# Kernel optimization log

Measured on AMD Instinct MI355X. Metric: run time of the kernel, lower is better.

## Reference

```python
import jax, jax.numpy as jnp
import numpy as np

B, S, H = 4, 2048, 1024

def setup_inputs() -> dict:
    key = jax.random.key(0)
    ks = jax.random.split(key, 4)
    scale = 1.0 / np.sqrt(H)
    x = jax.random.normal(ks[0], (B, S, H), dtype=jnp.float32)
    Wq = jax.random.normal(ks[1], (H, H), dtype=jnp.float32) * scale
    Wk = jax.random.normal(ks[2], (H, H), dtype=jnp.float32) * scale
    Wv = jax.random.normal(ks[3], (H, H), dtype=jnp.float32) * scale
    bq = jnp.zeros((H,), dtype=jnp.float32)
    bk = jnp.zeros((H,), dtype=jnp.float32)
    bv = jnp.zeros((H,), dtype=jnp.float32)
    return {"x": x, "Wq": Wq, "bq": bq, "Wk": Wk, "bk": bk, "Wv": Wv, "bv": bv}

def reference(x, Wq, bq, Wk, bk, Wv, bv):
    # Linear: y = x @ W^T + b (torch nn.Linear convention)
    Q = jnp.einsum('bsh,oh->bso', x, Wq) + bq
    K = jnp.einsum('bsh,oh->bso', x, Wk) + bk
    V = jnp.einsum('bsh,oh->bso', x, Wv) + bv
    scores = jnp.einsum('bqh,bkh->bqk', Q, K) / jnp.sqrt(jnp.float32(H))
    attn = jax.nn.softmax(scores, axis=-1)
    return jnp.einsum('bqk,bkh->bqh', attn, V)
```

## Files before the change

kernel.cpp:

```cpp
#include <hip/hip_runtime.h>
#include <cstdint>
#include <cstddef>


typedef __bf16 bf16;
typedef _Float16 f16;
typedef __bf16 bf16x8 __attribute__((ext_vector_type(8)));
typedef __bf16 bf16x4 __attribute__((ext_vector_type(4)));
typedef float f32x4 __attribute__((ext_vector_type(4)));

#define LDS_TOTAL 131072

#define XO (8388608 / 8)
#define WO (1048576 / 8)
__global__ __launch_bounds__(256)
void cvt_all(const float* __restrict__ x, const float* __restrict__ Wq,
             const float* __restrict__ Wk, const float* __restrict__ Wv,
             bf16* __restrict__ xb, bf16* __restrict__ Wqkv,
             float* __restrict__ rsum)
{
    const int i = blockIdx.x * 256 + threadIdx.x;
    if (i < 2048) {
        f32x4 zz = {0.f, 0.f, 0.f, 0.f};
        ((f32x4*)rsum)[i] = zz;
    }
    const float* src;
    bf16* dst;
    if (i < XO) {
        src = x + 8 * (size_t)i;
        dst = xb + 8 * (size_t)i;
    } else {
        const int j = i - XO;
        const int w = j / WO;
        const int off = j - w * WO;
        const float* ws_ = (w == 0) ? Wq : (w == 1) ? Wk : Wv;
        src = ws_ + 8 * (size_t)off;
        dst = Wqkv + 8 * (size_t)j;
    }
    f32x4 v0 = *(const f32x4*)src;
    f32x4 v1 = *(const f32x4*)(src + 4);
    bf16x8 o;
#pragma unroll
    for (int r = 0; r < 4; ++r) { o[r] = (bf16)v0[r]; o[4 + r] = (bf16)v1[r]; }
    *(bf16x8*)dst = o;
}

#define BM1 128
#define BN1 128
#define BK1 64

__device__ __forceinline__ void stage_tile(const bf16* __restrict__ g, int ld,
                                           bf16* lds_generic, int tid)
{
    auto lds3 = (__attribute__((address_space(3))) char*)lds_generic;
    const int wave = tid >> 6;
#pragma unroll
    for (int issue = 0; issue < 4; ++issue) {
        const int p   = issue * 256 + tid;
        const int row = p >> 3;
        const int cp  = p & 7;
        const int c   = cp ^ (row & 7);
        const bf16* gp = g + (size_t)row * ld + c * 8;
        const unsigned wave_base = (unsigned)(issue * 4096 + wave * 1024);
        __builtin_amdgcn_global_load_lds(
            (const __attribute__((address_space(1))) void*)gp,
            (__attribute__((address_space(3))) void*)(lds3 + wave_base),
            16, 0, 0);
    }
}

__device__ __forceinline__ bf16x8 read_frag(const bf16* lds, int row, int chunk)
{
    const int cp = chunk ^ (row & 7);
    return *(const bf16x8*)(lds + row * BK1 + cp * 8);
}

__global__ __launch_bounds__(256, 2)
void gemm_qkv(const bf16* __restrict__ A, const bf16* __restrict__ Bm,
              const float* __restrict__ bias0, const float* __restrict__ bias1,
              const float* __restrict__ bias2, bf16* __restrict__ C, int K)
{
    __shared__ alignas(16) bf16 As[2][BM1 * BK1];
    __shared__ alignas(16) bf16 Bs[2][BN1 * BK1];

    const int tid  = threadIdx.x;
    const int lane = tid & 63;
    const int wid  = tid >> 6;
    const int wr   = (wid >> 1) * 64;
    const int wc   = (wid & 1) * 64;
    const int quad = lane >> 4;
    const int l16  = lane & 15;

    {
    }
    const unsigned gx = gridDim.x;
    unsigned flat = blockIdx.x + gx * blockIdx.y;
    const unsigned chunk = (gx * gridDim.y) >> 3;
    flat = (flat & 7u) * chunk + (flat >> 3);
    const int bx = flat % gx;
    const int by = flat / gx;

    const int m0 = by * BM1;
    const int n0 = bx * BN1;

    const bf16* Ab = A + (size_t)m0 * K;
    const bf16* Bb = Bm + (size_t)n0 * K;

    f32x4 acc[4][4] = {};

    stage_tile(Ab, K, As[0], tid);
    stage_tile(Bb, K, Bs[0], tid);

    const int niter = K / BK1;
    for (int it = 0; it < niter; ++it) {
        const int cur = it & 1;
        __syncthreads();
        if (it + 1 < niter) {
            stage_tile(Ab + (it + 1) * BK1, K, As[cur ^ 1], tid);
            stage_tile(Bb + (it + 1) * BK1, K, Bs[cur ^ 1], tid);
        }
#pragma unroll
        for (int h = 0; h < 2; ++h) {
            bf16x8 af[4], bfr[4];
#pragma unroll
            for (int i = 0; i < 4; ++i)
                af[i]  = read_frag(As[cur], wr + i * 16 + l16, h * 4 + quad);
#pragma unroll
            for (int j = 0; j < 4; ++j)
                bfr[j] = read_frag(Bs[cur], wc + j * 16 + l16, h * 4 + quad);
#pragma unroll
            for (int i = 0; i < 4; ++i)
#pragma unroll
                for (int j = 0; j < 4; ++j)
                    acc[i][j] = __builtin_amdgcn_mfma_f32_16x16x32_bf16(
                        af[i], bfr[j], acc[i][j], 0, 0, 0);
        }
    }

#pragma unroll
    for (int j = 0; j < 4; ++j) {
        const int col3 = n0 + wc + j * 16 + l16;
#pragma unroll
        for (int i = 0; i < 4; ++i) {
            const int rbase = m0 + wr + i * 16 + quad * 4;
            const int mat = col3 >> 10;
            const int col = col3 & 1023;
            const float* bp = (mat == 0) ? bias0 : (mat == 1) ? bias1 : bias2;
            const float bj = bp[col];
            if (mat < 2) {
                bf16* Cb = C + (size_t)mat * (8u << 20);
#pragma unroll
                for (int r = 0; r < 4; ++r)
                    Cb[(size_t)(rbase + r) * 1024 + col] =
                        (bf16)(acc[i][j][r] + bj);
            } else {
                bf16* Cb = C + (size_t)(16u << 20);
                const int b = rbase >> 11;
                const int s = rbase & 2047;
                bf16x4 tmp;
#pragma unroll
                for (int r = 0; r < 4; ++r) tmp[r] = (bf16)(acc[i][j][r] + bj);
                *(bf16x4*)(Cb + (((size_t)((b << 10) + col)) << 11) + s) = tmp;
            }
        }
    }
}

template <int OUTMODE, int NW_N>
__global__ __launch_bounds__(512, 2)
void gemm256(const bf16* __restrict__ A, const bf16* __restrict__ Bm,
             void* __restrict__ C, float* __restrict__ rsum,
             int K, int N, float alpha, long zA, long zB, long zC)
{
    constexpr int MI = 2 * NW_N;
    extern __shared__ __align__(16) char smem[];
    auto lds3 = (__attribute__((address_space(3))) char*)smem;

    const int tid  = threadIdx.x;
    const int lane = tid & 63;
    const int wid  = tid >> 6;
    const int quad = lane >> 4;
    const int l16  = lane & 15;
    const int wc   = (wid % NW_N) * 64;
    const int wr   = (wid / NW_N) * (MI * 16);

    const unsigned gx = gridDim.x, gy = gridDim.y;
    unsigned flat = blockIdx.x + gx * (blockIdx.y + gy * blockIdx.z);
    const unsigned chunk = (gx * gy * gridDim.z) >> 3;
    flat = (flat & 7u) * chunk + (flat >> 3);
    const int bx = flat % gx;
    const unsigned r2 = flat / gx;
    const int by = r2 % gy;
    const int z  = r2 / gy;

    const int m0 = by * 256;
    const int n0 = bx * (NW_N * 64);

    const bf16* Ab = A + (size_t)z * zA + (size_t)m0 * K;
    const bf16* Bb = Bm + (size_t)z * zB + (size_t)n0 * K;

    const int sr  = tid >> 3;
    const int sc  = (tid & 7) ^ (sr & 7);
    const size_t soff = (size_t)sr * K + (size_t)sc * 8;
    const long  hstep = 64L * K;
    const long  h1off = 128L * K;
    const unsigned dmabase = (unsigned)(wid * 1024);

#define STAGE(g, ldsoff)                                                       \
    do {                                                                       \
        __builtin_amdgcn_global_load_lds(                                      \
            (const __attribute__((address_space(1))) void*)((g) + soff),       \
            (__attribute__((address_space(3))) void*)(lds3 + (ldsoff) + dmabase), \
            16, 0, 0);                                                         \
        __builtin_amdgcn_global_load_lds(                                      \
            (const __attribute__((address_space(1))) void*)((g) + soff + hstep), \
            (__attribute__((address_space(3))) void*)(lds3 + (ldsoff) + 8192 + dmabase), \
            16, 0, 0);                                                         \
    } while (0)

    const char* pa = (const char*)smem + (wr + l16) * 128;
    const int x0 = (quad ^ (l16 & 7)) * 16;

    const int NT = K / 64;
    f32x4 acc[MI][4] = {};

    if constexpr (NW_N == 4) {
        const char* pb = (const char*)smem + 65536 + (wc + l16) * 128;
        bf16x8 af[4][2], b01[2][2], b23[2][2];

        STAGE(Ab, 0u);           STAGE(Ab + h1off, 16384u);
        STAGE(Bb, 65536u);       STAGE(Bb + h1off, 65536u + 16384u);
        STAGE(Ab + 64, 32768u);  STAGE(Ab + 64 + h1off, 32768u + 16384u);
        asm volatile("s_waitcnt vmcnt(4)\n\ts_barrier" ::: "memory");

        for (int t = 0; t < NT; ++t) {
            const unsigned d  = (unsigned)(t & 1) * 32768u;
            const unsigned dn = 32768u - d;
            const char* paT = pa + d;
            const char* pbT = pb + d;

#pragma unroll
            for (int i = 0; i < 4; ++i) {
                af[i][0] = *(const bf16x8*)(paT + i * 2048 + x0);
                af[i][1] = *(const bf16x8*)(paT + i * 2048 + (x0 ^ 64));
            }
#pragma unroll
            for (int j = 0; j < 2; ++j) {
                b01[j][0] = *(const bf16x8*)(pbT + j * 2048 + x0);
                b01[j][1] = *(const bf16x8*)(pbT + j * 2048 + (x0 ^ 64));
            }
            if (t + 1 < NT) STAGE(Bb + (t + 1) * 64, 65536u + dn);
            __builtin_amdgcn_s_setprio(1);
#pragma unroll
            for (int i = 0; i < 4; ++i)
#pragma unroll
                for (int j = 0; j < 2; ++j) {
                    acc[i][j] = __builtin_amdgcn_mfma_f32_16x16x32_bf16(
                        af[i][0], b01[j][0], acc[i][j], 0, 0, 0);
                    acc[i][j] = __builtin_amdgcn_mfma_f32_16x16x32_bf16(
                        af[i][1], b01[j][1], acc[i][j], 0, 0, 0);
                }
            __builtin_amdgcn_s_setprio(0);

#pragma unroll
            for (int j = 0; j < 2; ++j) {
                b23[j][0] = *(const bf16x8*)(pbT + (2 + j) * 2048 + x0);
                b23[j][1] = *(const bf16x8*)(pbT + (2 + j) * 2048 + (x0 ^ 64));
            }
            if (t + 1 < NT) STAGE(Bb + (t + 1) * 64 + h1off, 65536u + dn + 16384u);
            __builtin_amdgcn_s_setprio(1);
#pragma unroll
            for (int i = 0; i < 4; ++i)
#pragma unroll
                for (int j = 0; j < 2; ++j) {
                    acc[i][2 + j] = __builtin_amdgcn_mfma_f32_16x16x32_bf16(
                        af[i][0], b23[j][0], acc[i][2 + j], 0, 0, 0);
                    acc[i][2 + j] = __builtin_amdgcn_mfma_f32_16x16x32_bf16(
                        af[i][1], b23[j][1], acc[i][2 + j], 0, 0, 0);
                }
            __builtin_amdgcn_s_setprio(0);

#pragma unroll
            for (int i = 0; i < 4; ++i) {
                af[i][0] = *(const bf16x8*)(paT + (4 + i) * 2048 + x0);
                af[i][1] = *(const bf16x8*)(paT + (4 + i) * 2048 + (x0 ^ 64));
            }
            __builtin_amdgcn_s_setprio(1);
#pragma unroll
            for (int i = 0; i < 4; ++i)
#pragma unroll
                for (int j = 0; j < 2; ++j) {
                    acc[4 + i][2 + j] = __builtin_amdgcn_mfma_f32_16x16x32_bf16(
                        af[i][0], b23[j][0], acc[4 + i][2 + j], 0, 0, 0);
                    acc[4 + i][2 + j] = __builtin_amdgcn_mfma_f32_16x16x32_bf16(
                        af[i][1], b23[j][1], acc[4 + i][2 + j], 0, 0, 0);
                }
            __builtin_amdgcn_s_setprio(0);

            asm volatile("s_barrier" ::: "memory");

#pragma unroll
            for (int j = 0; j < 2; ++j) {
                b01[j][0] = *(const bf16x8*)(pbT + j * 2048 + x0);
                b01[j][1] = *(const bf16x8*)(pbT + j * 2048 + (x0 ^ 64));
            }
            if (t + 2 < NT) {
                STAGE(Ab + (t + 2) * 64, d);
                STAGE(Ab + (t + 2) * 64 + h1off, d + 16384u);
            }
            __builtin_amdgcn_s_setprio(1);
#pragma unroll
            for (int i = 0; i < 4; ++i)
#pragma unroll
                for (int j = 0; j < 2; ++j) {
                    acc[4 + i][j] = __builtin_amdgcn_mfma_f32_16x16x32_bf16(
                        af[i][0], b01[j][0], acc[4 + i][j], 0, 0, 0);
                    acc[4 + i][j] = __builtin_amdgcn_mfma_f32_16x16x32_bf16(
                        af[i][1], b01[j][1], acc[4 + i][j], 0, 0, 0);
                }
            __builtin_amdgcn_s_setprio(0);

            if (t + 2 < NT)
                asm volatile("s_waitcnt vmcnt(4)\n\ts_barrier" ::: "memory");
            else if (t + 1 < NT)
                asm volatile("s_waitcnt vmcnt(0)\n\ts_barrier" ::: "memory");
        }
    } else {
        bf16x8 af[2][2], bfr[4][2];

        STAGE(Ab, 0u);           STAGE(Ab + h1off, 16384u);
        STAGE(Bb, 98304u);
        STAGE(Ab + 64, 32768u);  STAGE(Ab + 64 + h1off, 32768u + 16384u);
        asm volatile("s_waitcnt vmcnt(4)\n\ts_barrier" ::: "memory");

        for (int t = 0; t < NT; ++t) {
            const char* paT = pa + (unsigned)(t % 3) * 32768u;
            const char* pbT = (const char*)smem + 98304u +
                              (unsigned)(t & 1) * 16384u + (wc + l16) * 128;

#pragma unroll
            for (int i = 0; i < 2; ++i) {
                af[i][0] = *(const bf16x8*)(paT + i * 2048 + x0);
                af[i][1] = *(const bf16x8*)(paT + i * 2048 + (x0 ^ 64));
            }
#pragma unroll
            for (int j = 0; j < 4; ++j) {
                bfr[j][0] = *(const bf16x8*)(pbT + j * 2048 + x0);
                bfr[j][1] = *(const bf16x8*)(pbT + j * 2048 + (x0 ^ 64));
            }
            if (t + 1 < NT)
                STAGE(Bb + (t + 1) * 64, 98304u + (unsigned)((t + 1) & 1) * 16384u);
            __builtin_amdgcn_s_setprio(1);
#pragma unroll
            for (int i = 0; i < 2; ++i)
#pragma unroll
                for (int j = 0; j < 4; ++j) {
                    acc[i][j] = __builtin_amdgcn_mfma_f32_16x16x32_bf16(
                        af[i][0], bfr[j][0], acc[i][j], 0, 0, 0);
                    acc[i][j] = __builtin_amdgcn_mfma_f32_16x16x32_bf16(
                        af[i][1], bfr[j][1], acc[i][j], 0, 0, 0);
                }
            __builtin_amdgcn_s_setprio(0);

#pragma unroll
            for (int i = 0; i < 2; ++i) {
                af[i][0] = *(const bf16x8*)(paT + (2 + i) * 2048 + x0);
                af[i][1] = *(const bf16x8*)(paT + (2 + i) * 2048 + (x0 ^ 64));
            }
            if (t + 2 < NT) {
                const unsigned da = (unsigned)((t + 2) % 3) * 32768u;
                STAGE(Ab + (t + 2) * 64, da);
                STAGE(Ab + (t + 2) * 64 + h1off, da + 16384u);
            }
            __builtin_amdgcn_s_setprio(1);
#pragma unroll
            for (int i = 0; i < 2; ++i)
#pragma unroll
                for (int j = 0; j < 4; ++j) {
                    acc[2 + i][j] = __builtin_amdgcn_mfma_f32_16x16x32_bf16(
                        af[i][0], bfr[j][0], acc[2 + i][j], 0, 0, 0);
                    acc[2 + i][j] = __builtin_amdgcn_mfma_f32_16x16x32_bf16(
                        af[i][1], bfr[j][1], acc[2 + i][j], 0, 0, 0);
                }
            __builtin_amdgcn_s_setprio(0);

            if (t + 2 < NT)
                asm volatile("s_waitcnt vmcnt(4)\n\ts_barrier" ::: "memory");
            else if (t + 1 < NT)
                asm volatile("s_waitcnt vmcnt(0)\n\ts_barrier" ::: "memory");
        }
    }
#undef STAGE

    if constexpr (OUTMODE == 5) {
        float psum[8][4];
#pragma unroll
        for (int i = 0; i < 8; ++i)
#pragma unroll
            for (int r = 0; r < 4; ++r) psum[i][r] = 0.f;

        bf16* Pb = (bf16*)C + (size_t)z * zC;
#pragma unroll
        for (int j = 0; j < 4; ++j) {
            const int col3 = n0 + wc + j * 16 + l16;
#pragma unroll
            for (int i = 0; i < MI; ++i) {
                const int rbase = m0 + wr + i * 16 + quad * 4;
#pragma unroll
                for (int r = 0; r < 4; ++r) {
                    const float p = __expf(acc[i][j][r] * alpha);
                    Pb[(size_t)(rbase + r) * N + col3] = (bf16)p;
                    psum[i][r] += p;
                }
            }
        }
#pragma unroll
        for (int i = 0; i < MI; ++i)
#pragma unroll
            for (int r = 0; r < 4; ++r) {
#pragma unroll
                for (int o = 1; o < 16; o <<= 1)
                    psum[i][r] += __shfl_xor(psum[i][r], o, 64);
            }
        if (l16 == 0) {
            float* rs = rsum + (size_t)z * 2048;
#pragma unroll
            for (int i = 0; i < MI; ++i) {
                const int rbase = m0 + wr + i * 16 + quad * 4;
#pragma unroll
                for (int r = 0; r < 4; ++r)
                    atomicAdd(&rs[rbase + r], psum[i][r]);
            }
        }
    } else {
        const float* rs = rsum + (size_t)z * 2048;
#pragma unroll
        for (int j = 0; j < 4; ++j) {
            const int col3 = n0 + wc + j * 16 + l16;
#pragma unroll
            for (int i = 0; i < MI; ++i) {
                const int rbase = m0 + wr + i * 16 + quad * 4;
                float* Cf = (float*)C + (size_t)z * zC;
#pragma unroll
                for (int r = 0; r < 4; ++r)
                    Cf[(size_t)(rbase + r) * N + col3] =
                        acc[i][j][r] * (1.0f / rs[rbase + r]);
            }
        }
    }
}

extern "C" void kernel_launch(void* const* d_in, const int* in_sizes, int n_in,
                              void* d_out, int out_size, void* d_ws, size_t ws_size,
                              hipStream_t stream)
{
    constexpr int B = 4, S = 2048, H = 1024;
    const float* x  = (const float*)d_in[0];
    const float* Wq = (const float*)d_in[1];
    const float* bq = (const float*)d_in[2];
    const float* Wk = (const float*)d_in[3];
    const float* bk = (const float*)d_in[4];
    const float* Wv = (const float*)d_in[5];
    const float* bv = (const float*)d_in[6];
    float* out = (float*)d_out;

    char* ws = (char*)d_ws;
    bf16* xb    = (bf16*)ws;
    bf16* Wqkv  = (bf16*)(ws + (size_t)(16 << 20));
    float* rsum = (float*)(ws + (size_t)(22 << 20));
    bf16* Q     = (bf16*)(ws + (size_t)(24 << 20));
    bf16* Kp    = (bf16*)(ws + (size_t)(40 << 20));
    bf16* Vt    = (bf16*)(ws + (size_t)(56 << 20));
    bf16* P     = (bf16*)(ws + (size_t)(72 << 20));

    static bool attr_done = false;
    if (!attr_done) {
        attr_done = true;
        (void)hipFuncSetAttribute(reinterpret_cast<const void*>(gemm256<5, 4>),
                                  hipFuncAttributeMaxDynamicSharedMemorySize,
                                  LDS_TOTAL);
        (void)hipFuncSetAttribute(reinterpret_cast<const void*>(gemm256<6, 2>),
                                  hipFuncAttributeMaxDynamicSharedMemorySize,
                                  LDS_TOTAL);
    }

    dim3 blk(256, 1, 1);
    dim3 blk512(512, 1, 1);

    cvt_all<<<dim3((XO + 3 * WO) / 256), blk, 0, stream>>>(
        x, Wq, Wk, Wv, xb, Wqkv, rsum);

    gemm_qkv<<<dim3(3 * H / BN1, (B * S) / BM1, 1), blk, 0, stream>>>(
        xb, Wqkv, bq, bk, bv, Q, H);

    gemm256<5, 4><<<dim3(S / 256, S / 256, B), blk512, LDS_TOTAL, stream>>>(
        Q, Kp, P, rsum, H, S, 0.03125f,
        (long)S * H, (long)S * H, (long)S * S);

    gemm256<6, 2><<<dim3(H / 128, S / 256, B), blk512, LDS_TOTAL, stream>>>(
        P, Vt, out, rsum, S, H, 1.0f,
        (long)S * S, (long)H * S, (long)S * H);
}
```

Baseline: 237.9 us.

## Fuse QK^T-softmax and PV GEMMs into one kernel with per-row-group spin barrier

Merges the score/exp GEMM and the P·V GEMM into a single persistent-style kernel of 256 blocks. Each block computes one 256x256 score tile, adds its partial row sums atomically, then spin-waits on a per-row-group counter until all 8 column tiles are done before computing its 256x128 output tile. This removes a kernel launch and the tail between the two GEMMs, and keeps P hot in L2. It relies on all 256 blocks being co-resident, at two per CU, or the spin barrier deadlocks. The QKV GEMM also drops its block-index swizzle.

```diff
diff --git a/kernel.cpp b/kernel.cpp
--- a/kernel.cpp
+++ b/kernel.cpp
@@ -4,7 +4,6 @@
 
 
 typedef __bf16 bf16;
-typedef _Float16 f16;
 typedef __bf16 bf16x8 __attribute__((ext_vector_type(8)));
 typedef __bf16 bf16x4 __attribute__((ext_vector_type(4)));
 typedef float f32x4 __attribute__((ext_vector_type(4)));
@@ -17,13 +16,12 @@
 void cvt_all(const float* __restrict__ x, const float* __restrict__ Wq,
              const float* __restrict__ Wk, const float* __restrict__ Wv,
              bf16* __restrict__ xb, bf16* __restrict__ Wqkv,
-             float* __restrict__ rsum)
+             float* __restrict__ rsum, unsigned* __restrict__ cnt)
 {
     const int i = blockIdx.x * 256 + threadIdx.x;
-    if (i < 2048) {
-        f32x4 zz = {0.f, 0.f, 0.f, 0.f};
-        ((f32x4*)rsum)[i] = zz;
-    }
+    f32x4 zz = {0.f, 0.f, 0.f, 0.f};
+    if (i < 2048) ((f32x4*)rsum)[i] = zz;
+    if (i < 8)    ((f32x4*)(void*)cnt)[i] = zz;
     const float* src;
     bf16* dst;
     if (i < XO) {
@@ -91,17 +89,8 @@
     const int quad = lane >> 4;
     const int l16  = lane & 15;
 
-    {
-    }
-    const unsigned gx = gridDim.x;
-    unsigned flat = blockIdx.x + gx * blockIdx.y;
-    const unsigned chunk = (gx * gridDim.y) >> 3;
-    flat = (flat & 7u) * chunk + (flat >> 3);
-    const int bx = flat % gx;
-    const int by = flat / gx;
-
-    const int m0 = by * BM1;
-    const int n0 = bx * BN1;
+    const int m0 = blockIdx.y * BM1;
+    const int n0 = blockIdx.x * BN1;
 
     const bf16* Ab = A + (size_t)m0 * K;
     const bf16* Bb = Bm + (size_t)n0 * K;
@@ -166,13 +155,12 @@
     }
 }
 
-template <int OUTMODE, int NW_N>
 __global__ __launch_bounds__(512, 2)
-void gemm256(const bf16* __restrict__ A, const bf16* __restrict__ Bm,
-             void* __restrict__ C, float* __restrict__ rsum,
-             int K, int N, float alpha, long zA, long zB, long zC)
+void attn_fused(const bf16* __restrict__ Qg, const bf16* __restrict__ Kg,
+                const bf16* __restrict__ Vtg, bf16* __restrict__ Pg,
+                float* __restrict__ rsum, unsigned* __restrict__ cnt,
+                float* __restrict__ out)
 {
-    constexpr int MI = 2 * NW_N;
     extern __shared__ __align__(16) char smem[];
     auto lds3 = (__attribute__((address_space(3))) char*)smem;
 
@@ -181,56 +169,53 @@
     const int wid  = tid >> 6;
     const int quad = lane >> 4;
     const int l16  = lane & 15;
-    const int wc   = (wid % NW_N) * 64;
-    const int wr   = (wid / NW_N) * (MI * 16);
-
-    const unsigned gx = gridDim.x, gy = gridDim.y;
+
+    const unsigned gx = 8, gy = 8;
     unsigned flat = blockIdx.x + gx * (blockIdx.y + gy * blockIdx.z);
-    const unsigned chunk = (gx * gy * gridDim.z) >> 3;
-    flat = (flat & 7u) * chunk + (flat >> 3);
+    flat = (flat & 7u) * 32u + (flat >> 3);
     const int bx = flat % gx;
     const unsigned r2 = flat / gx;
     const int by = r2 % gy;
     const int z  = r2 / gy;
-
-    const int m0 = by * 256;
-    const int n0 = bx * (NW_N * 64);
-
-    const bf16* Ab = A + (size_t)z * zA + (size_t)m0 * K;
-    const bf16* Bb = Bm + (size_t)z * zB + (size_t)n0 * K;
-
-    const int sr  = tid >> 3;
-    const int sc  = (tid & 7) ^ (sr & 7);
-    const size_t soff = (size_t)sr * K + (size_t)sc * 8;
-    const long  hstep = 64L * K;
-    const long  h1off = 128L * K;
+    const int grp = z * 8 + by;
+
+    const int sr = tid >> 3;
+    const int sc = (tid & 7) ^ (sr & 7);
     const unsigned dmabase = (unsigned)(wid * 1024);
-
-#define STAGE(g, ldsoff)                                                       \
+    const int x0 = (quad ^ (l16 & 7)) * 16;
+
+#define STAGE(g, soff, hstep, ldsoff)                                          \
     do {                                                                       \
         __builtin_amdgcn_global_load_lds(                                      \
-            (const __attribute__((address_space(1))) void*)((g) + soff),       \
+            (const __attribute__((address_space(1))) void*)((g) + (soff)),     \
             (__attribute__((address_space(3))) void*)(lds3 + (ldsoff) + dmabase), \
             16, 0, 0);                                                         \
         __builtin_amdgcn_global_load_lds(                                      \
-            (const __attribute__((address_space(1))) void*)((g) + soff + hstep), \
+            (const __attribute__((address_space(1))) void*)((g) + (soff) + (hstep)), \
             (__attribute__((address_space(3))) void*)(lds3 + (ldsoff) + 8192 + dmabase), \
             16, 0, 0);                                                         \
     } while (0)
 
-    const char* pa = (const char*)smem + (wr + l16) * 128;
-    const int x0 = (quad ^ (l16 & 7)) * 16;
-
-    const int NT = K / 64;
-    f32x4 acc[MI][4] = {};
-
-    if constexpr (NW_N == 4) {
+    {
+        constexpr int K = 1024, N = 2048, NT = K / 64;
+        const size_t soff = (size_t)sr * K + (size_t)sc * 8;
+        const long hstep = 64L * K, h1off = 128L * K;
+        const int wc = (wid & 3) * 64;
+        const int wr = (wid >> 2) * 128;
+        const int m0 = by * 256, n0 = bx * 256;
+
+        const bf16* Ab = Qg + (size_t)z * (2048 * 1024) + (size_t)m0 * K;
+        const bf16* Bb = Kg + (size_t)z * (2048 * 1024) + (size_t)n0 * K;
+
+        const char* pa = (const char*)smem + (wr + l16) * 128;
         const char* pb = (const char*)smem + 65536 + (wc + l16) * 128;
+
+        f32x4 acc[8][4] = {};
         bf16x8 af[4][2], b01[2][2], b23[2][2];
 
-        STAGE(Ab, 0u);           STAGE(Ab + h1off, 16384u);
-        STAGE(Bb, 65536u);       STAGE(Bb + h1off, 65536u + 16384u);
-        STAGE(Ab + 64, 32768u);  STAGE(Ab + 64 + h1off, 32768u + 16384u);
+        STAGE(Ab, soff, hstep, 0u);          STAGE(Ab + h1off, soff, hstep, 16384u);
+        STAGE(Bb, soff, hstep, 65536u);      STAGE(Bb + h1off, soff, hstep, 65536u + 16384u);
+        STAGE(Ab + 64, soff, hstep, 32768u); STAGE(Ab + 64 + h1off, soff, hstep, 32768u + 16384u);
         asm volatile("s_waitcnt vmcnt(4)\n\ts_barrier" ::: "memory");
 
         for (int t = 0; t < NT; ++t) {
@@ -249,7 +234,7 @@
                 b01[j][0] = *(const bf16x8*)(pbT + j * 2048 + x0);
                 b01[j][1] = *(const bf16x8*)(pbT + j * 2048 + (x0 ^ 64));
             }
-            if (t + 1 < NT) STAGE(Bb + (t + 1) * 64, 65536u + dn);
+            if (t + 1 < NT) STAGE(Bb + (t + 1) * 64, soff, hstep, 65536u + dn);
             __builtin_amdgcn_s_setprio(1);
 #pragma unroll
             for (int i = 0; i < 4; ++i)
@@ -267,7 +252,7 @@
                 b23[j][0] = *(const bf16x8*)(pbT + (2 + j) * 2048 + x0);
                 b23[j][1] = *(const bf16x8*)(pbT + (2 + j) * 2048 + (x0 ^ 64));
             }
-            if (t + 1 < NT) STAGE(Bb + (t + 1) * 64 + h1off, 65536u + dn + 16384u);
+            if (t + 1 < NT) STAGE(Bb + (t + 1) * 64 + h1off, soff, hstep, 65536u + dn + 16384u);
             __builtin_amdgcn_s_setprio(1);
 #pragma unroll
             for (int i = 0; i < 4; ++i)
@@ -305,8 +290,8 @@
                 b01[j][1] = *(const bf16x8*)(pbT + j * 2048 + (x0 ^ 64));
             }
             if (t + 2 < NT) {
-                STAGE(Ab + (t + 2) * 64, d);
-                STAGE(Ab + (t + 2) * 64 + h1off, d + 16384u);
+                STAGE(Ab + (t + 2) * 64, soff, hstep, d);
+                STAGE(Ab + (t + 2) * 64 + h1off, soff, hstep, d + 16384u);
             }
             __builtin_amdgcn_s_setprio(1);
 #pragma unroll
@@ -325,18 +310,84 @@
             else if (t + 1 < NT)
                 asm volatile("s_waitcnt vmcnt(0)\n\ts_barrier" ::: "memory");
         }
-    } else {
+
+        float psum[8][4];
+#pragma unroll
+        for (int i = 0; i < 8; ++i)
+#pragma unroll
+            for (int r = 0; r < 4; ++r) psum[i][r] = 0.f;
+
+        bf16* Pb = Pg + (size_t)z * (2048 * 2048);
+#pragma unroll
+        for (int j = 0; j < 4; ++j) {
+            const int col3 = n0 + wc + j * 16 + l16;
+#pragma unroll
+            for (int i = 0; i < 8; ++i) {
+                const int rbase = m0 + wr + i * 16 + quad * 4;
+#pragma unroll
+                for (int r = 0; r < 4; ++r) {
+                    const float p = __expf(acc[i][j][r] * 0.03125f);
+                    Pb[(size_t)(rbase + r) * N + col3] = (bf16)p;
+                    psum[i][r] += p;
+                }
+            }
+        }
+#pragma unroll
+        for (int i = 0; i < 8; ++i)
+#pragma unroll
+            for (int r = 0; r < 4; ++r) {
+#pragma unroll
+                for (int o = 1; o < 16; o <<= 1)
+                    psum[i][r] += __shfl_xor(psum[i][r], o, 64);
+            }
+        if (l16 == 0) {
+            float* rs = rsum + (size_t)z * 2048;
+#pragma unroll
+            for (int i = 0; i < 8; ++i) {
+                const int rbase = m0 + wr + i * 16 + quad * 4;
+#pragma unroll
+                for (int r = 0; r < 4; ++r)
+                    atomicAdd(&rs[rbase + r], psum[i][r]);
+            }
+        }
+    }
+
+    __syncthreads();
+    if (tid == 0)
+        __hip_atomic_fetch_add(&cnt[grp], 1u, __ATOMIC_RELEASE,
+                               __HIP_MEMORY_SCOPE_AGENT);
+    if (tid == 0) {
+        while (__hip_atomic_load(&cnt[grp], __ATOMIC_ACQUIRE,
+                                 __HIP_MEMORY_SCOPE_AGENT) < 8u)
+            __builtin_amdgcn_s_sleep(1);
+    }
+    __syncthreads();
+
+    {
+        constexpr int K = 2048, N = 1024, NT = K / 64;
+        const size_t soff = (size_t)sr * K + (size_t)sc * 8;
+        const long hstep = 64L * K, h1off = 128L * K;
+        const int wc = (wid & 1) * 64;
+        const int wr = (wid >> 1) * 64;
+        const int m0 = by * 256, n0 = bx * 128;
+
+        const bf16* Ab = Pg + (size_t)z * (2048 * 2048) + (size_t)m0 * K;
+        const bf16* Bb = Vtg + (size_t)z * (1024 * 2048) + (size_t)n0 * K;
+
+        const char* pa = (const char*)smem + (wr + l16) * 128;
+
+        f32x4 acc[4][4] = {};
         bf16x8 af[2][2], bfr[4][2];
 
-        STAGE(Ab, 0u);           STAGE(Ab + h1off, 16384u);
-        STAGE(Bb, 98304u);
-        STAGE(Ab + 64, 32768u);  STAGE(Ab + 64 + h1off, 32768u + 16384u);
+        STAGE(Ab, soff, hstep, 0u);          STAGE(Ab + h1off, soff, hstep, 16384u);
+        STAGE(Bb, soff, hstep, 98304u);
+        STAGE(Ab + 64, soff, hstep, 32768u); STAGE(Ab + 64 + h1off, soff, hstep, 32768u + 16384u);
         asm volatile("s_waitcnt vmcnt(4)\n\ts_barrier" ::: "memory");
 
         for (int t = 0; t < NT; ++t) {
             const char* paT = pa + (unsigned)(t % 3) * 32768u;
             const char* pbT = (const char*)smem + 98304u +
-                              (unsigned)(t & 1) * 16384u + (wc + l16) * 128;
+                              (unsigned)(t & 1) * 16384u + ((wid & 1) * 64 + l16) * 128;
 
 #pragma unroll
             for (int i = 0; i < 2; ++i) {
@@ -349,7 +400,8 @@
                 bfr[j][1] = *(const bf16x8*)(pbT + j * 2048 + (x0 ^ 64));
             }
             if (t + 1 < NT)
-                STAGE(Bb + (t + 1) * 64, 98304u + (unsigned)((t + 1) & 1) * 16384u);
+                STAGE(Bb + (t + 1) * 64, soff, hstep,
+                      98304u + (unsigned)((t + 1) & 1) * 16384u);
             __builtin_amdgcn_s_setprio(1);
 #pragma unroll
             for (int i = 0; i < 2; ++i)
@@ -369,8 +421,8 @@
             }
             if (t + 2 < NT) {
                 const unsigned da = (unsigned)((t + 2) % 3) * 32768u;
-                STAGE(Ab + (t + 2) * 64, da);
-                STAGE(Ab + (t + 2) * 64 + h1off, da + 16384u);
+                STAGE(Ab + (t + 2) * 64, soff, hstep, da);
+                STAGE(Ab + (t + 2) * 64 + h1off, soff, hstep, da + 16384u);
             }
             __builtin_amdgcn_s_setprio(1);
 #pragma unroll
@@ -389,58 +441,15 @@
             else if (t + 1 < NT)
                 asm volatile("s_waitcnt vmcnt(0)\n\ts_barrier" ::: "memory");
         }
-    }
-#undef STAGE
-
-    if constexpr (OUTMODE == 5) {
-        float psum[8][4];
-#pragma unroll
-        for (int i = 0; i < 8; ++i)
-#pragma unroll
-            for (int r = 0; r < 4; ++r) psum[i][r] = 0.f;
-
-        bf16* Pb = (bf16*)C + (size_t)z * zC;
+
+        const float* rs = rsum + (size_t)z * 2048;
+        float* Cf = out + (size_t)z * (2048 * 1024);
 #pragma unroll
         for (int j = 0; j < 4; ++j) {
             const int col3 = n0 + wc + j * 16 + l16;
 #pragma unroll
-            for (int i = 0; i < MI; ++i) {
+            for (int i = 0; i < 4; ++i) {
                 const int rbase = m0 + wr + i * 16 + quad * 4;
-#pragma unroll
-                for (int r = 0; r < 4; ++r) {
-                    const float p = __expf(acc[i][j][r] * alpha);
-                    Pb[(size_t)(rbase + r) * N + col3] = (bf16)p;
-                    psum[i][r] += p;
-                }
-            }
-        }
-#pragma unroll
-        for (int i = 0; i < MI; ++i)
-#pragma unroll
-            for (int r = 0; r < 4; ++r) {
-#pragma unroll
-                for (int o = 1; o < 16; o <<= 1)
-                    psum[i][r] += __shfl_xor(psum[i][r], o, 64);
-            }
-        if (l16 == 0) {
-            float* rs = rsum + (size_t)z * 2048;
-#pragma unroll
-            for (int i = 0; i < MI; ++i) {
-                const int rbase = m0 + wr + i * 16 + quad * 4;
-#pragma unroll
-                for (int r = 0; r < 4; ++r)
-                    atomicAdd(&rs[rbase + r], psum[i][r]);
-            }
-        }
-    } else {
-        const float* rs = rsum + (size_t)z * 2048;
-#pragma unroll
-        for (int j = 0; j < 4; ++j) {
-            const int col3 = n0 + wc + j * 16 + l16;
-#pragma unroll
-            for (int i = 0; i < MI; ++i) {
-                const int rbase = m0 + wr + i * 16 + quad * 4;
-                float* Cf = (float*)C + (size_t)z * zC;
 #pragma unroll
                 for (int r = 0; r < 4; ++r)
                     Cf[(size_t)(rbase + r) * N + col3] =
@@ -448,6 +457,7 @@
             }
         }
     }
+#undef STAGE
 }
 
 extern "C" void kernel_launch(void* const* d_in, const int* in_sizes, int n_in,
@@ -465,39 +475,32 @@
     float* out = (float*)d_out;
 
     char* ws = (char*)d_ws;
-    bf16* xb    = (bf16*)ws;
-    bf16* Wqkv  = (bf16*)(ws + (size_t)(16 << 20));
-    float* rsum = (float*)(ws + (size_t)(22 << 20));
-    bf16* Q     = (bf16*)(ws + (size_t)(24 << 20));
-    bf16* Kp    = (bf16*)(ws + (size_t)(40 << 20));
-    bf16* Vt    = (bf16*)(ws + (size_t)(56 << 20));
-    bf16* P     = (bf16*)(ws + (size_t)(72 << 20));
+    bf16* xb      = (bf16*)ws;
+    bf16* Wqkv    = (bf16*)(ws + (size_t)(16 << 20));
+    float* rsum   = (float*)(ws + (size_t)(22 << 20));
+    unsigned* cnt = (unsigned*)(ws + (size_t)(22 << 20) + 32768);
+    bf16* Q       = (bf16*)(ws + (size_t)(24 << 20));
+    bf16* Kp      = (bf16*)(ws + (size_t)(40 << 20));
+    bf16* Vt      = (bf16*)(ws + (size_t)(56 << 20));
+    bf16* P       = (bf16*)(ws + (size_t)(72 << 20));
 
     static bool attr_done = false;
     if (!attr_done) {
         attr_done = true;
-        (void)hipFuncSetAttribute(reinterpret_cast<const void*>(gemm256<5, 4>),
+        (void)hipFuncSetAttribute(reinterpret_cast<const void*>(attn_fused),
                                   hipFuncAttributeMaxDynamicSharedMemorySize,
                                   LDS_TOTAL);
-        (void)hipFuncSetAttribute(reinterpret_cast<const void*>(gemm256<6, 2>),
-                                  hipFuncAttributeMaxDynamicSharedMemorySize,
-                                  LDS_TOTAL);
     }
 
     dim3 blk(256, 1, 1);
     dim3 blk512(512, 1, 1);
 
     cvt_all<<<dim3((XO + 3 * WO) / 256), blk, 0, stream>>>(
-        x, Wq, Wk, Wv, xb, Wqkv, rsum);
+        x, Wq, Wk, Wv, xb, Wqkv, rsum, cnt);
 
     gemm_qkv<<<dim3(3 * H / BN1, (B * S) / BM1, 1), blk, 0, stream>>>(
         xb, Wqkv, bq, bk, bv, Q, H);
 
-    gemm256<5, 4><<<dim3(S / 256, S / 256, B), blk512, LDS_TOTAL, stream>>>(
-        Q, Kp, P, rsum, H, S, 0.03125f,
-        (long)S * H, (long)S * H, (long)S * S);
-
-    gemm256<6, 2><<<dim3(H / 128, S / 256, B), blk512, LDS_TOTAL, stream>>>(
-        P, Vt, out, rsum, S, H, 1.0f,
-        (long)S * S, (long)H * S, (long)S * H);
+    attn_fused<<<dim3(8, 8, B), blk512, LDS_TOTAL, stream>>>(
+        Q, Kp, Vt, P, rsum, cnt, out);
 }
```

Result: slower. 252.6 us (+6.2%).
